# Optimization experiments

Measured on AMD Instinct MI355X. Metric: run time of the kernel, lower is better.

Reference implementation:

```python
import jax, jax.numpy as jnp
import numpy as np

B, N1, N2, D = 8, 2048, 2048, 512


def setup_inputs() -> dict:
    key = jax.random.key(0)
    k1, k2, k3 = jax.random.split(key, 3)
    matrix_1 = jax.random.normal(k1, (B, N1, D), dtype=jnp.float32)
    matrix_2 = jax.random.normal(k2, (B, N2, D), dtype=jnp.float32)
    # Linear similarity with combination 'x,y': weight over concat([x, y]) -> size 2*D
    weight = jax.random.normal(k3, (2 * D,), dtype=jnp.float32) * (1.0 / np.sqrt(2 * D))
    bias = jnp.zeros((1,), dtype=jnp.float32)
    return {"matrix_1": matrix_1, "matrix_2": matrix_2, "weight": weight, "bias": bias}


def reference(matrix_1, matrix_2, weight, bias):
    # Faithful to MatrixAttention + default Linear similarity:
    # sim[b,i,j] = dot(weight, concat(matrix_1[b,i], matrix_2[b,j])) + bias
    # The original tiles both matrices to (B, N1, N2, D); mathematically this
    # factors into two projections plus a broadcast add (same math, no tiling).
    d = matrix_1.shape[-1]
    w1, w2 = weight[:d], weight[d:]
    s1 = jnp.einsum('bnd,d->bn', matrix_1, w1)  # (B, N1)
    s2 = jnp.einsum('bmd,d->bm', matrix_2, w2)  # (B, N2)
    return s1[:, :, None] + s2[:, None, :] + bias[0]  # (B, N1, N2)
```

## Files before the change

kernel.cpp:

```cpp
#include <hip/hip_runtime.h>


#define DDIM 512
#define BB   8
#define NN   2048
#define ROWS (BB * NN)
#define RPW  4
#define WROWS  8
#define MCHUNK 512

typedef float f32x4 __attribute__((ext_vector_type(4)));

__global__ __launch_bounds__(256) void dot_kernel(const float* __restrict__ m1,
                                                  const float* __restrict__ m2,
                                                  const float* __restrict__ w,
                                                  float* __restrict__ s) {
    int wave  = (int)((blockIdx.x * blockDim.x + threadIdx.x) >> 6);
    int lane  = threadIdx.x & 63;
    int vrow0 = wave * RPW;

    const float* src;
    const float* wp;
    int row0;
    if (vrow0 < ROWS) { src = m1; wp = w;        row0 = vrow0; }
    else              { src = m2; wp = w + DDIM; row0 = vrow0 - ROWS; }

    const f32x4* wv = reinterpret_cast<const f32x4*>(wp);
    f32x4 w0 = wv[lane];
    f32x4 w1 = wv[lane + 64];

    f32x4 a0[RPW], a1[RPW];
    #pragma unroll
    for (int r = 0; r < RPW; ++r) {
        const f32x4* rp = reinterpret_cast<const f32x4*>(src + (size_t)(row0 + r) * DDIM);
        a0[r] = rp[lane];
        a1[r] = rp[lane + 64];
    }

    float acc[RPW];
    #pragma unroll
    for (int r = 0; r < RPW; ++r) {
        acc[r] = a0[r].x * w0.x + a0[r].y * w0.y + a0[r].z * w0.z + a0[r].w * w0.w
               + a1[r].x * w1.x + a1[r].y * w1.y + a1[r].z * w1.z + a1[r].w * w1.w;
    }

    #pragma unroll
    for (int r = 0; r < RPW; ++r) {
        #pragma unroll
        for (int off = 1; off < 64; off <<= 1)
            acc[r] += __shfl_xor(acc[r], off, 64);
    }

    if (lane == 0) {
        #pragma unroll
        for (int r = 0; r < RPW; ++r)
            s[vrow0 + r] = acc[r];
    }
}

__global__ __launch_bounds__(256) void add_kernel(const float* __restrict__ s1,
                                                  const float* __restrict__ s2,
                                                  const float* __restrict__ bias,
                                                  float* __restrict__ out) {
    int wave = (int)((blockIdx.x * blockDim.x + threadIdx.x) >> 6);
    int lane = threadIdx.x & 63;
    int m_chunk = wave & (NN / MCHUNK - 1);
    int bn      = wave >> 2;
    int n0      = (bn & (NN / WROWS - 1)) * WROWS;
    int b       = bn >> 8;

    const float bval = bias[0];

    const f32x4* s2v = reinterpret_cast<const f32x4*>(s2 + (size_t)b * NN + m_chunk * MCHUNK);
    f32x4 v2a = s2v[lane];
    f32x4 v2b = s2v[lane + 64];

    const float* s1p = s1 + (size_t)b * NN + n0;
    float* op = out + ((size_t)(b * NN + n0)) * NN + m_chunk * MCHUNK;

    #pragma unroll
    for (int r = 0; r < WROWS; ++r) {
        float v1 = s1p[r] + bval;
        f32x4* orow = reinterpret_cast<f32x4*>(op + (size_t)r * NN);
        orow[lane]      = v2a + v1;
        orow[lane + 64] = v2b + v1;
    }
}

extern "C" void kernel_launch(void* const* d_in, const int* in_sizes, int n_in,
                              void* d_out, int out_size, void* d_ws, size_t ws_size,
                              hipStream_t stream) {
    const float* m1   = (const float*)d_in[0];
    const float* m2   = (const float*)d_in[1];
    const float* w    = (const float*)d_in[2];
    const float* bias = (const float*)d_in[3];
    float* out = (float*)d_out;

    float* s  = (float*)d_ws;
    float* s1 = s;
    float* s2 = s + ROWS;

    dot_kernel<<<(2 * ROWS) / (RPW * 4), 256, 0, stream>>>(m1, m2, w, s);

    add_kernel<<<2048, 256, 0, stream>>>(s1, s2, bias, out);
}
```

Before: 36.52 us.

## Fuse matrix_1 projection into broadcast-add output kernel

The first kernel now computes only the matrix_2 projection. The second kernel computes each matrix_1 row dot product itself and writes the full output rows straight away, so s1 is no longer written to and read back from workspace. Each wave holds all of the batch's s2 (2048 floats, 32 VGPRs) in registers and writes 4 full output rows. The gain is a smaller first kernel and less workspace traffic, but register pressure rises and the output store pattern changes.

Measured after the change: 36.20 us, median of 2. Within noise of the previous version (-0.9%).

```diff
diff --git a/kernel.cpp b/kernel.cpp
--- a/kernel.cpp
+++ b/kernel.cpp
@@ -6,43 +6,33 @@
 #define NN   2048
 #define ROWS (BB * NN)
 #define RPW  4
-#define WROWS  8
-#define MCHUNK 512
 
 typedef float f32x4 __attribute__((ext_vector_type(4)));
 
-__global__ __launch_bounds__(256) void dot_kernel(const float* __restrict__ m1,
-                                                  const float* __restrict__ m2,
-                                                  const float* __restrict__ w,
-                                                  float* __restrict__ s) {
-    int wave  = (int)((blockIdx.x * blockDim.x + threadIdx.x) >> 6);
-    int lane  = threadIdx.x & 63;
-    int vrow0 = wave * RPW;
+__global__ __launch_bounds__(256) void dot2_kernel(const float* __restrict__ m2,
+                                                   const float* __restrict__ w,
+                                                   float* __restrict__ s2) {
+    int wave = (int)((blockIdx.x * blockDim.x + threadIdx.x) >> 6);
+    int lane = threadIdx.x & 63;
+    int row0 = wave * RPW;
 
-    const float* src;
-    const float* wp;
-    int row0;
-    if (vrow0 < ROWS) { src = m1; wp = w;        row0 = vrow0; }
-    else              { src = m2; wp = w + DDIM; row0 = vrow0 - ROWS; }
-
-    const f32x4* wv = reinterpret_cast<const f32x4*>(wp);
+    const f32x4* wv = reinterpret_cast<const f32x4*>(w + DDIM);
     f32x4 w0 = wv[lane];
     f32x4 w1 = wv[lane + 64];
 
     f32x4 a0[RPW], a1[RPW];
     #pragma unroll
     for (int r = 0; r < RPW; ++r) {
-        const f32x4* rp = reinterpret_cast<const f32x4*>(src + (size_t)(row0 + r) * DDIM);
+        const f32x4* rp = reinterpret_cast<const f32x4*>(m2 + (size_t)(row0 + r) * DDIM);
         a0[r] = rp[lane];
         a1[r] = rp[lane + 64];
     }
 
     float acc[RPW];
     #pragma unroll
-    for (int r = 0; r < RPW; ++r) {
+    for (int r = 0; r < RPW; ++r)
         acc[r] = a0[r].x * w0.x + a0[r].y * w0.y + a0[r].z * w0.z + a0[r].w * w0.w
                + a1[r].x * w1.x + a1[r].y * w1.y + a1[r].z * w1.z + a1[r].w * w1.w;
-    }
 
     #pragma unroll
     for (int r = 0; r < RPW; ++r) {
@@ -54,36 +44,59 @@
     if (lane == 0) {
         #pragma unroll
         for (int r = 0; r < RPW; ++r)
-            s[vrow0 + r] = acc[r];
+            s2[row0 + r] = acc[r];
     }
 }
 
-__global__ __launch_bounds__(256) void add_kernel(const float* __restrict__ s1,
-                                                  const float* __restrict__ s2,
-                                                  const float* __restrict__ bias,
-                                                  float* __restrict__ out) {
+__global__ __launch_bounds__(256) void fused_kernel(const float* __restrict__ m1,
+                                                    const float* __restrict__ w,
+                                                    const float* __restrict__ s2,
+                                                    const float* __restrict__ bias,
+                                                    float* __restrict__ out) {
     int wave = (int)((blockIdx.x * blockDim.x + threadIdx.x) >> 6);
     int lane = threadIdx.x & 63;
-    int m_chunk = wave & (NN / MCHUNK - 1);
-    int bn      = wave >> 2;
-    int n0      = (bn & (NN / WROWS - 1)) * WROWS;
-    int b       = bn >> 8;
+    int row0 = wave * RPW;
+    int b    = row0 >> 11;
+
+    const f32x4* wv = reinterpret_cast<const f32x4*>(w);
+    f32x4 w0 = wv[lane];
+    f32x4 w1 = wv[lane + 64];
+
+    f32x4 a0[RPW], a1[RPW];
+    #pragma unroll
+    for (int r = 0; r < RPW; ++r) {
+        const f32x4* rp = reinterpret_cast<const f32x4*>(m1 + (size_t)(row0 + r) * DDIM);
+        a0[r] = rp[lane];
+        a1[r] = rp[lane + 64];
+    }
+
+    const f32x4* s2v = reinterpret_cast<const f32x4*>(s2 + (size_t)b * NN);
+    f32x4 v2[NN / 4 / 64];
+    #pragma unroll
+    for (int k = 0; k < NN / 4 / 64; ++k)
+        v2[k] = s2v[lane + 64 * k];
+
+    float acc[RPW];
+    #pragma unroll
+    for (int r = 0; r < RPW; ++r)
+        acc[r] = a0[r].x * w0.x + a0[r].y * w0.y + a0[r].z * w0.z + a0[r].w * w0.w
+               + a1[r].x * w1.x + a1[r].y * w1.y + a1[r].z * w1.z + a1[r].w * w1.w;
+
+    #pragma unroll
+    for (int r = 0; r < RPW; ++r) {
+        #pragma unroll
+        for (int off = 1; off < 64; off <<= 1)
+            acc[r] += __shfl_xor(acc[r], off, 64);
+    }
 
     const float bval = bias[0];
-
-    const f32x4* s2v = reinterpret_cast<const f32x4*>(s2 + (size_t)b * NN + m_chunk * MCHUNK);
-    f32x4 v2a = s2v[lane];
-    f32x4 v2b = s2v[lane + 64];
-
-    const float* s1p = s1 + (size_t)b * NN + n0;
-    float* op = out + ((size_t)(b * NN + n0)) * NN + m_chunk * MCHUNK;
-
     #pragma unroll
-    for (int r = 0; r < WROWS; ++r) {
-        float v1 = s1p[r] + bval;
-        f32x4* orow = reinterpret_cast<f32x4*>(op + (size_t)r * NN);
-        orow[lane]      = v2a + v1;
-        orow[lane + 64] = v2b + v1;
+    for (int r = 0; r < RPW; ++r) {
+        float v1 = acc[r] + bval;
+        f32x4* orow = reinterpret_cast<f32x4*>(out + (size_t)(row0 + r) * NN);
+        #pragma unroll
+        for (int k = 0; k < NN / 4 / 64; ++k)
+            orow[lane + 64 * k] = v2[k] + v1;
     }
 }
 
@@ -95,12 +108,9 @@
     const float* w    = (const float*)d_in[2];
     const float* bias = (const float*)d_in[3];
     float* out = (float*)d_out;
+    float* s2  = (float*)d_ws;
 
-    float* s  = (float*)d_ws;
-    float* s1 = s;
-    float* s2 = s + ROWS;
+    dot2_kernel<<<ROWS / (RPW * 4), 256, 0, stream>>>(m2, w, s2);
 
-    dot_kernel<<<(2 * ROWS) / (RPW * 4), 256, 0, stream>>>(m1, m2, w, s);
-
-    add_kernel<<<2048, 256, 0, stream>>>(s1, s2, bias, out);
+    fused_kernel<<<ROWS / (RPW * 4), 256, 0, stream>>>(m1, w, s2, bias, out);
 }
```
